# Kernel tuning notes

Measured on AMD Instinct MI355X. Metric: run time of the kernel, lower is better.

The kernel has to match this reference:

```python
import jax, jax.numpy as jnp
import numpy as np

K = 3          # kernel size
STRIDE = 1
PAD = 1
DIL = 1


def setup_inputs() -> dict:
    key = jax.random.key(0)
    k1, k2, k3 = jax.random.split(key, 3)
    N, Cin, H, W = 8, 128, 64, 64
    Cout = 128
    x = jax.random.normal(k1, (N, Cin, H, W), dtype=jnp.float32)
    # offset channels: 2 * deformable_groups * K*K = 18, interleaved (dy, dx) per tap
    offset = jax.random.normal(k2, (N, 2 * K * K, H, W), dtype=jnp.float32)
    weight = jax.random.normal(k3, (Cout, Cin, K, K), dtype=jnp.float32) / np.sqrt(Cin * K * K)
    return {"x": x, "offset": offset, "weight": weight}


def _deform_conv(x, offset, weight):
    N, Cin, H, W = x.shape
    Cout = weight.shape[0]
    KK = K * K
    Ho, Wo = offset.shape[2], offset.shape[3]

    off = offset.reshape(N, KK, 2, Ho, Wo)
    dy = off[:, :, 0]  # [N, KK, Ho, Wo]
    dx = off[:, :, 1]

    kh = jnp.repeat(jnp.arange(K), K).astype(x.dtype)   # [KK]
    kw = jnp.tile(jnp.arange(K), K).astype(x.dtype)     # [KK]
    base_i = (jnp.arange(Ho) * STRIDE - PAD).astype(x.dtype)  # [Ho]
    base_j = (jnp.arange(Wo) * STRIDE - PAD).astype(x.dtype)  # [Wo]

    # Sampling positions: [N, KK, Ho, Wo]
    py = base_i[None, None, :, None] + (kh * DIL)[None, :, None, None] + dy
    px = base_j[None, None, None, :] + (kw * DIL)[None, :, None, None] + dx

    y0 = jnp.floor(py)
    x0 = jnp.floor(px)
    wy1 = py - y0
    wx1 = px - x0
    wy0 = 1.0 - wy1
    wx0 = 1.0 - wx1
    y0i = y0.astype(jnp.int32)
    x0i = x0.astype(jnp.int32)
    y1i = y0i + 1
    x1i = x0i + 1

    x_flat = x.reshape(N, Cin, H * W)

    def gather(yi, xi):
        # zero-padding outside the image
        mask = ((yi >= 0) & (yi < H) & (xi >= 0) & (xi < W)).astype(x.dtype)
        idx = jnp.clip(yi, 0, H - 1) * W + jnp.clip(xi, 0, W - 1)  # [N,KK,Ho,Wo]
        v = jnp.take_along_axis(x_flat, idx.reshape(N, 1, -1), axis=2)  # [N,Cin,KK*Ho*Wo]
        v = v.reshape(N, Cin, KK, Ho, Wo)
        return v * mask[:, None]

    sampled = (gather(y0i, x0i) * (wy0 * wx0)[:, None]
               + gather(y0i, x1i) * (wy0 * wx1)[:, None]
               + gather(y1i, x0i) * (wy1 * wx0)[:, None]
               + gather(y1i, x1i) * (wy1 * wx1)[:, None])  # [N,Cin,KK,Ho,Wo]

    w = weight.reshape(Cout, Cin, KK)
    return jnp.einsum('nckij,ock->noij', sampled, w)


def reference(x, offset, weight):
    return _deform_conv(x, offset, weight)
```

## Files before the change

### kernel.cpp

```cpp
#include <hip/hip_runtime.h>


#define H  64
#define W  64
#define CIN 128
#define COUT 128
#define NB 8
#define KK 9
#define SROW (CIN + 8)

typedef short bf16x8 __attribute__((ext_vector_type(8)));
typedef float f32x4  __attribute__((ext_vector_type(4)));

#define GLD4(dst, voff, base, IMM) \
    asm volatile("global_load_dwordx4 %0, %1, %2 offset:" IMM \
                 : "=v"(dst) : "v"(voff), "s"(base))
#define GLD1(dst, voff, base) \
    asm volatile("global_load_dword %0, %1, %2" \
                 : "=v"(dst) : "v"(voff), "s"(base))
#define DRAIN() { asm volatile("s_waitcnt vmcnt(0)" ::: "memory"); \
                  __builtin_amdgcn_sched_barrier(0); }

__device__ __forceinline__ unsigned short f2bf(float f) {
    unsigned u = __builtin_bit_cast(unsigned, f);
    u += 0x7FFFu + ((u >> 16) & 1u);
    return (unsigned short)(u >> 16);
}
__device__ __forceinline__ unsigned cvt_pk_bf16(float lo, float hi) {
    unsigned r;
    asm("v_cvt_pk_bf16_f32 %0, %1, %2" : "=v"(r) : "v"(lo), "v"(hi));
    return r;
}
__device__ __forceinline__ float lo_f(unsigned u) { return __builtin_bit_cast(float, u << 16); }
__device__ __forceinline__ float hi_f(unsigned u) { return __builtin_bit_cast(float, u & 0xFFFF0000u); }

__global__ void prep_all(const float* __restrict__ x, const float* __restrict__ w,
                         unsigned short* __restrict__ xt, unsigned short* __restrict__ wt) {
    int b = blockIdx.x;
    int t = threadIdx.x;
    if (b >= NB * H) {
        int idx = (b - NB * H) * 256 + t;
        if (idx < KK * COUT * CIN) {
            int e  = idx & 7;
            int lq = (idx >> 3) & 3;
            int lm = (idx >> 5) & 15;
            int ct = (idx >> 9) & 3;
            int nt = (idx >> 11) & 1;
            int c4 = (idx >> 12) & 3;
            int kk = idx >> 14;
            int co = (c4 << 5) + (nt << 4) + lm;
            int ch = (ct << 5) + (lq << 3) + e;
            wt[idx] = f2bf(w[(co * CIN + ch) * KK + kk]);
        }
        return;
    }
    __shared__ float tile[CIN][W + 4];
    int n = b & 7, y = b >> 3;
    const float* src = x + ((size_t)n * CIN * H + y) * W;
    #pragma unroll
    for (int it = 0; it < 8; ++it) {
        int idx = it * 256 + t;
        int c  = idx >> 4;
        int x4 = (idx & 15) << 2;
        int xs = (x4 + ((c >> 5) << 4)) & 63;
        *(float4*)&tile[c][xs] = *(const float4*)(src + (size_t)c * H * W + x4);
    }
    __syncthreads();
    int xp = t >> 2;
    int cbch = (t & 3) << 5;
    int xr = (xp + ((cbch >> 5) << 4)) & 63;
    unsigned short* dst = xt + (((size_t)(n * H + y) * W + xp) * CIN + cbch);
    unsigned rr[16];
    #pragma unroll
    for (int i = 0; i < 16; ++i)
        rr[i] = cvt_pk_bf16(tile[cbch + 2 * i][xr], tile[cbch + 2 * i + 1][xr]);
    #pragma unroll
    for (int i = 0; i < 4; ++i)
        ((uint4*)dst)[i] = make_uint4(rr[4*i], rr[4*i+1], rr[4*i+2], rr[4*i+3]);
}

__global__ __launch_bounds__(512, 2) void fused_main(
        const float* __restrict__ offs, const unsigned short* __restrict__ xt,
        const unsigned short* __restrict__ wt, float* __restrict__ out) {
    __shared__ __attribute__((aligned(16))) unsigned short samp[2][64][SROW];

    int b = blockIdx.x;
    int n = b & 7, ho = b >> 3;
    int t = threadIdx.x;
    int lane = t & 63, wv = t >> 6;
    int lm = lane & 15, lq = lane >> 4;

    int pos = t >> 3;
    int cb  = (t & 7) << 4;
    int cb2 = cb << 1;

    const float* offs_b = offs + (size_t)(n * 2 * KK) * H * W + (size_t)ho * W;
    const unsigned short* xt_b = xt + (size_t)n * H * W * CIN;

    float dyv[KK], dxv[KK];
    #pragma unroll
    for (int tap = 0; tap < KK; ++tap) {
        GLD1(dyv[tap], (unsigned)(((2 * tap) * H * W + pos) * 4), offs_b);
        GLD1(dxv[tap], (unsigned)(((2 * tap + 1) * H * W + pos) * 4), offs_b);
    }
    DRAIN();

    unsigned vo[KK][4];
    float bw[KK][4];
    #pragma unroll
    for (int tap = 0; tap < KK; ++tap) {
        float py = (float)(ho - 1 + tap / 3) + dyv[tap];
        float px = (float)(pos - 1 + tap % 3) + dxv[tap];
        float y0f = floorf(py), x0f = floorf(px);
        float wy1 = py - y0f, wx1 = px - x0f;
        float wy0 = 1.f - wy1, wx0 = 1.f - wx1;
        int y0 = (int)y0f, x0 = (int)x0f;
        int y1 = y0 + 1, x1 = x0 + 1;
        bool vy0 = (unsigned)y0 < (unsigned)H, vy1 = (unsigned)y1 < (unsigned)H;
        bool vx0 = (unsigned)x0 < (unsigned)W, vx1 = (unsigned)x1 < (unsigned)W;
        bw[tap][0] = (vy0 && vx0) ? wy0 * wx0 : 0.f;
        bw[tap][1] = (vy0 && vx1) ? wy0 * wx1 : 0.f;
        bw[tap][2] = (vy1 && vx0) ? wy1 * wx0 : 0.f;
        bw[tap][3] = (vy1 && vx1) ? wy1 * wx1 : 0.f;
        int yc0 = min(max(y0, 0), H - 1), yc1 = min(max(y1, 0), H - 1);
        int xc0 = min(max(x0, 0), W - 1), xc1 = min(max(x1, 0), W - 1);
        vo[tap][0] = (unsigned)((yc0 << 14) + (xc0 << 8) + cb2);
        vo[tap][1] = (unsigned)((yc0 << 14) + (xc1 << 8) + cb2);
        vo[tap][2] = (unsigned)((yc1 << 14) + (xc0 << 8) + cb2);
        vo[tap][3] = (unsigned)((yc1 << 14) + (xc1 << 8) + cb2);
    }

    unsigned stash[KK][8];
    #pragma unroll
    for (int grp = 0; grp < 3; ++grp) {
        uint4 gq[3][8];
        #pragma unroll
        for (int i = 0; i < 3; ++i) {
            int tap = grp * 3 + i;
            GLD4(gq[i][0], vo[tap][0], xt_b, "0");
            GLD4(gq[i][1], vo[tap][0], xt_b, "16");
            GLD4(gq[i][2], vo[tap][1], xt_b, "0");
            GLD4(gq[i][3], vo[tap][1], xt_b, "16");
            GLD4(gq[i][4], vo[tap][2], xt_b, "0");
            GLD4(gq[i][5], vo[tap][2], xt_b, "16");
            GLD4(gq[i][6], vo[tap][3], xt_b, "0");
            GLD4(gq[i][7], vo[tap][3], xt_b, "16");
        }
        DRAIN();
        #pragma unroll
        for (int i = 0; i < 3; ++i) {
            int tap = grp * 3 + i;
            float w00 = bw[tap][0], w01 = bw[tap][1], w10 = bw[tap][2], w11 = bw[tap][3];
            #pragma unroll
            for (int h = 0; h < 2; ++h) {
                const unsigned* a0 = (const unsigned*)&gq[i][0 + h];
                const unsigned* a1 = (const unsigned*)&gq[i][2 + h];
                const unsigned* a2 = (const unsigned*)&gq[i][4 + h];
                const unsigned* a3 = (const unsigned*)&gq[i][6 + h];
                #pragma unroll
                for (int q = 0; q < 4; ++q) {
                    float v0 = w00*lo_f(a0[q]) + w01*lo_f(a1[q]) + w10*lo_f(a2[q]) + w11*lo_f(a3[q]);
                    float v1 = w00*hi_f(a0[q]) + w01*hi_f(a1[q]) + w10*hi_f(a2[q]) + w11*hi_f(a3[q]);
                    stash[tap][4*h + q] = cvt_pk_bf16(v0, v1);
                }
            }
        }
    }

    f32x4 acc[4];
    #pragma unroll
    for (int mt = 0; mt < 4; ++mt) acc[mt] = f32x4{0.f, 0.f, 0.f, 0.f};

    int slot = (lm << 2) + lq;
    const unsigned short* wvbase = wt + ((size_t)wv << 11) + (slot << 3);

    {
        unsigned short* ld = &samp[0][pos][cb];
        *(uint4*)(ld)     = make_uint4(stash[0][0], stash[0][1], stash[0][2], stash[0][3]);
        *(uint4*)(ld + 8) = make_uint4(stash[0][4], stash[0][5], stash[0][6], stash[0][7]);
    }
    __syncthreads();

    #pragma unroll
    for (int tap = 0; tap < KK; ++tap) {
        if (tap < KK - 1) {
            unsigned short* ld = &samp[(tap + 1) & 1][pos][cb];
            *(uint4*)(ld)     = make_uint4(stash[tap+1][0], stash[tap+1][1],
                                           stash[tap+1][2], stash[tap+1][3]);
            *(uint4*)(ld + 8) = make_uint4(stash[tap+1][4], stash[tap+1][5],
                                           stash[tap+1][6], stash[tap+1][7]);
        }
        const unsigned short* wkb = wvbase + ((size_t)(tap << 3) << 11);
        bf16x8 bW[4];
        #pragma unroll
        for (int ct = 0; ct < 4; ++ct)
            bW[ct] = *(const bf16x8*)(wkb + (ct << 9));

        __builtin_amdgcn_s_setprio(1);
        #pragma unroll
        for (int ct = 0; ct < 4; ++ct) {
            bf16x8 a[4];
            #pragma unroll
            for (int mt = 0; mt < 4; ++mt)
                a[mt] = *(const bf16x8*)&samp[tap & 1][lm + (mt << 4)][(ct << 5) + (lq << 3)];
            #pragma unroll
            for (int mt = 0; mt < 4; ++mt)
                acc[mt] = __builtin_amdgcn_mfma_f32_16x16x32_bf16(a[mt], bW[ct], acc[mt], 0, 0, 0);
        }
        __builtin_amdgcn_s_setprio(0);
        __syncthreads();
    }

    int co = (wv << 4) + lm;
    #pragma unroll
    for (int mt = 0; mt < 4; ++mt) {
        int wob = (mt << 4) + (lq << 2);
        *(f32x4*)(out + (((size_t)(n * COUT + co) * H + ho) * W + wob)) = acc[mt];
    }
}

extern "C" void kernel_launch(void* const* d_in, const int* in_sizes, int n_in,
                              void* d_out, int out_size, void* d_ws, size_t ws_size,
                              hipStream_t stream) {
    const float* x      = (const float*)d_in[0];
    const float* offset = (const float*)d_in[1];
    const float* weight = (const float*)d_in[2];
    float* out = (float*)d_out;

    unsigned short* xt = (unsigned short*)d_ws;
    unsigned short* wt = (unsigned short*)((char*)d_ws + 8388608);

    int wblocks = (KK * COUT * CIN + 255) / 256;
    hipLaunchKernelGGL(prep_all, dim3(NB * H + wblocks), dim3(256), 0, stream,
                       x, weight, xt, wt);
    hipLaunchKernelGGL(fused_main, dim3(NB * H), dim3(512), 0, stream,
                       offset, xt, wt, out);
}
```

Before: 109.4 us.

## Stage all nine taps in LDS and retile waves as 2x2 MFMA blocks

Bilinear samples for all nine taps are written straight into a nine-slot shared-memory buffer, replacing the per-tap register stash and the double-buffered LDS loop. A single barrier replaces the nine per-tap ones. Each wave now computes a 2x2 grid of 16x16 tiles (half the output positions, 32 output channels), so it reuses each A and B fragment twice. The shared buffer grows to about 150 KB, which likely allows only one 512-thread block per CU instead of the two the launch bounds request. The row stride of 132 elements also breaks 16-byte alignment of the vector LDS accesses, which may be slow or unsafe.

```diff
diff --git a/kernel.cpp b/kernel.cpp
--- a/kernel.cpp
+++ b/kernel.cpp
@@ -7,7 +7,7 @@
 #define COUT 128
 #define NB 8
 #define KK 9
-#define SROW (CIN + 8)
+#define SROW4 132
 
 typedef short bf16x8 __attribute__((ext_vector_type(8)));
 typedef float f32x4  __attribute__((ext_vector_type(4)));
@@ -82,7 +82,7 @@
 __global__ __launch_bounds__(512, 2) void fused_main(
         const float* __restrict__ offs, const unsigned short* __restrict__ xt,
         const unsigned short* __restrict__ wt, float* __restrict__ out) {
-    __shared__ __attribute__((aligned(16))) unsigned short samp[2][64][SROW];
+    __shared__ __attribute__((aligned(16))) unsigned short samp[KK][64][SROW4];
 
     int b = blockIdx.x;
     int n = b & 7, ho = b >> 3;
@@ -130,7 +130,6 @@
         vo[tap][3] = (unsigned)((yc1 << 14) + (xc1 << 8) + cb2);
     }
 
-    unsigned stash[KK][8];
     #pragma unroll
     for (int grp = 0; grp < 3; ++grp) {
         uint4 gq[3][8];
@@ -151,6 +150,7 @@
         for (int i = 0; i < 3; ++i) {
             int tap = grp * 3 + i;
             float w00 = bw[tap][0], w01 = bw[tap][1], w10 = bw[tap][2], w11 = bw[tap][3];
+            unsigned rr[8];
             #pragma unroll
             for (int h = 0; h < 2; ++h) {
                 const unsigned* a0 = (const unsigned*)&gq[i][0 + h];
@@ -161,61 +161,61 @@
                 for (int q = 0; q < 4; ++q) {
                     float v0 = w00*lo_f(a0[q]) + w01*lo_f(a1[q]) + w10*lo_f(a2[q]) + w11*lo_f(a3[q]);
                     float v1 = w00*hi_f(a0[q]) + w01*hi_f(a1[q]) + w10*hi_f(a2[q]) + w11*hi_f(a3[q]);
-                    stash[tap][4*h + q] = cvt_pk_bf16(v0, v1);
+                    rr[4*h + q] = cvt_pk_bf16(v0, v1);
                 }
             }
-        }
-    }
-
-    f32x4 acc[4];
-    #pragma unroll
-    for (int mt = 0; mt < 4; ++mt) acc[mt] = f32x4{0.f, 0.f, 0.f, 0.f};
-
+            unsigned short* ld = &samp[tap][pos][cb];
+            *(uint4*)(ld)     = make_uint4(rr[0], rr[1], rr[2], rr[3]);
+            *(uint4*)(ld + 8) = make_uint4(rr[4], rr[5], rr[6], rr[7]);
+        }
+    }
+
+    __syncthreads();
+
+    int ph2 = wv & 1;
+    int cq  = wv >> 1;
     int slot = (lm << 2) + lq;
-    const unsigned short* wvbase = wt + ((size_t)wv << 11) + (slot << 3);
-
-    {
-        unsigned short* ld = &samp[0][pos][cb];
-        *(uint4*)(ld)     = make_uint4(stash[0][0], stash[0][1], stash[0][2], stash[0][3]);
-        *(uint4*)(ld + 8) = make_uint4(stash[0][4], stash[0][5], stash[0][6], stash[0][7]);
-    }
-    __syncthreads();
+
+    f32x4 acc[2][2];
+    #pragma unroll
+    for (int mt = 0; mt < 2; ++mt)
+        #pragma unroll
+        for (int nt = 0; nt < 2; ++nt) acc[mt][nt] = f32x4{0.f, 0.f, 0.f, 0.f};
+
+    const unsigned short* wq = wt + ((size_t)cq << 12) + (slot << 3);
 
     #pragma unroll
     for (int tap = 0; tap < KK; ++tap) {
-        if (tap < KK - 1) {
-            unsigned short* ld = &samp[(tap + 1) & 1][pos][cb];
-            *(uint4*)(ld)     = make_uint4(stash[tap+1][0], stash[tap+1][1],
-                                           stash[tap+1][2], stash[tap+1][3]);
-            *(uint4*)(ld + 8) = make_uint4(stash[tap+1][4], stash[tap+1][5],
-                                           stash[tap+1][6], stash[tap+1][7]);
-        }
-        const unsigned short* wkb = wvbase + ((size_t)(tap << 3) << 11);
-        bf16x8 bW[4];
-        #pragma unroll
-        for (int ct = 0; ct < 4; ++ct)
-            bW[ct] = *(const bf16x8*)(wkb + (ct << 9));
-
-        __builtin_amdgcn_s_setprio(1);
+        const unsigned short* wkb = wq + ((size_t)(tap << 2) << 12);
+        bf16x8 bW[2][4];
+        #pragma unroll
+        for (int nt = 0; nt < 2; ++nt)
+            #pragma unroll
+            for (int ct = 0; ct < 4; ++ct)
+                bW[nt][ct] = *(const bf16x8*)(wkb + (nt << 11) + (ct << 9));
+
         #pragma unroll
         for (int ct = 0; ct < 4; ++ct) {
-            bf16x8 a[4];
-            #pragma unroll
-            for (int mt = 0; mt < 4; ++mt)
-                a[mt] = *(const bf16x8*)&samp[tap & 1][lm + (mt << 4)][(ct << 5) + (lq << 3)];
-            #pragma unroll
-            for (int mt = 0; mt < 4; ++mt)
-                acc[mt] = __builtin_amdgcn_mfma_f32_16x16x32_bf16(a[mt], bW[ct], acc[mt], 0, 0, 0);
-        }
-        __builtin_amdgcn_s_setprio(0);
-        __syncthreads();
-    }
-
-    int co = (wv << 4) + lm;
-    #pragma unroll
-    for (int mt = 0; mt < 4; ++mt) {
-        int wob = (mt << 4) + (lq << 2);
-        *(f32x4*)(out + (((size_t)(n * COUT + co) * H + ho) * W + wob)) = acc[mt];
+            bf16x8 a[2];
+            #pragma unroll
+            for (int mt = 0; mt < 2; ++mt)
+                a[mt] = *(const bf16x8*)&samp[tap][(ph2 << 5) + (mt << 4) + lm][(ct << 5) + (lq << 3)];
+            #pragma unroll
+            for (int mt = 0; mt < 2; ++mt)
+                #pragma unroll
+                for (int nt = 0; nt < 2; ++nt)
+                    acc[mt][nt] = __builtin_amdgcn_mfma_f32_16x16x32_bf16(a[mt], bW[nt][ct], acc[mt][nt], 0, 0, 0);
+        }
+    }
+
+    #pragma unroll
+    for (int mt = 0; mt < 2; ++mt) {
+        int wob = (ph2 << 5) + (mt << 4) + (lq << 2);
+        #pragma unroll
+        for (int nt = 0; nt < 2; ++nt) {
+            int co = (cq << 5) + (nt << 4) + lm;
+            *(f32x4*)(out + (((size_t)(n * COUT + co) * H + ho) * W + wob)) = acc[mt][nt];
+        }
     }
 }
 
```

New measurement: 112.8 us. 3.1% more time.
